# Optimization experiments

Hardware: AMD Instinct MI355X
Metric: run time of the kernel (lower is better)

The kernel has to match this reference:

```python
import jax, jax.numpy as jnp
import numpy as np

BETA = 0.25


def setup_inputs() -> dict:
    key = jax.random.key(0)
    k1, k2 = jax.random.split(key)
    x = jax.random.normal(k1, (32768, 512), dtype=jnp.float32)
    centroids = jax.random.normal(k2, (8192, 512), dtype=jnp.float32)
    return {"x": x, "centroids": centroids}


def reference(x, centroids):
    # x: [N, D], centroids: [K, D]
    x_norm = jnp.sum(x * x, axis=1, keepdims=True)          # [N, 1]
    c_norm = jnp.sum(centroids * centroids, axis=1)         # [K]
    xy = jnp.einsum('nd,kd->nk', x, centroids)              # [N, K]
    distances = x_norm + c_norm[None, :] - 2.0 * xy         # [N, K]
    indices = jnp.argmin(distances, axis=-1)                # [N]
    q = centroids[indices]                                  # [N, D] gather
    # losses: commitment = mse(sg(q), x); codebook = mse(q, sg(x))
    sg = jax.lax.stop_gradient
    commitment_loss = jnp.mean((sg(q) - x) ** 2)
    codebook_loss = jnp.mean((q - sg(x)) ** 2)
    loss = codebook_loss + BETA * commitment_loss
    # straight-through estimator
    x_q = x + sg(q - x)
    return (x_q, loss, indices)
```

## Files before the change

kernel.cpp:

```cpp
#include <hip/hip_runtime.h>
#include <hip/hip_bf16.h>

#define N_ROWS 32768
#define DIM    512
#define K_CENT 8192

#define LOSS_OFF 16777216u
#define IDX_OFF  16777217u

#define XH_OFF_B   0u
#define CH_OFF_B   33554432u
#define CN_OFF_B   41943040u
#define CAND_OFF_B 41975808u

#define BM   128
#define BN   128
#define KHALF 4096
#define NKT  (KHALF / BN)

typedef __bf16 bf16x8 __attribute__((ext_vector_type(8)));
typedef float  f32x4  __attribute__((ext_vector_type(4)));

__device__ __forceinline__ unsigned short f2bf(float f) {
    unsigned u = __float_as_uint(f);
    return (unsigned short)((u + 0x7fffu + ((u >> 16) & 1u)) >> 16);
}

__device__ __forceinline__ void glds16(void* lds, const void* g) {
    __builtin_amdgcn_global_load_lds(
        (const __attribute__((address_space(1))) unsigned*)g,
        (__attribute__((address_space(3))) unsigned*)lds, 16, 0, 0);
}

__global__ void __launch_bounds__(256) convert_kernel(const float* __restrict__ x,
                                                      const float* __restrict__ c,
                                                      unsigned short* __restrict__ xh,
                                                      unsigned short* __restrict__ ch,
                                                      float* __restrict__ cnp) {
    const int wave = threadIdx.x >> 6, lane = threadIdx.x & 63;
    const int gid = blockIdx.x * 4 + wave;
    if (gid < N_ROWS) {
        const float* p = x + (size_t)gid * DIM + lane * 8;
        float4 a = *(const float4*)p, b = *(const float4*)(p + 4);
        uint4 w;
        w.x = (unsigned)f2bf(a.x) | ((unsigned)f2bf(a.y) << 16);
        w.y = (unsigned)f2bf(a.z) | ((unsigned)f2bf(a.w) << 16);
        w.z = (unsigned)f2bf(b.x) | ((unsigned)f2bf(b.y) << 16);
        w.w = (unsigned)f2bf(b.z) | ((unsigned)f2bf(b.w) << 16);
        *(uint4*)(xh + (size_t)gid * DIM + lane * 8) = w;
    } else {
        const int cr = gid - N_ROWS;
        const float* p = c + (size_t)cr * DIM + lane * 8;
        float4 a = *(const float4*)p, b = *(const float4*)(p + 4);
        uint4 w;
        w.x = (unsigned)f2bf(a.x) | ((unsigned)f2bf(a.y) << 16);
        w.y = (unsigned)f2bf(a.z) | ((unsigned)f2bf(a.w) << 16);
        w.z = (unsigned)f2bf(b.x) | ((unsigned)f2bf(b.y) << 16);
        w.w = (unsigned)f2bf(b.z) | ((unsigned)f2bf(b.w) << 16);
        *(uint4*)(ch + (size_t)cr * DIM + lane * 8) = w;
        float s = a.x*a.x + a.y*a.y + a.z*a.z + a.w*a.w
                + b.x*b.x + b.y*b.y + b.z*b.z + b.w*b.w;
#pragma unroll
        for (int off = 32; off; off >>= 1) s += __shfl_down(s, off, 64);
        if (lane == 0) cnp[cr] = s;
    }
}

__device__ __forceinline__ void ce(float& da, int& ia, float& db, int& ib) {
    bool sw = (db < da) || (db == da && ib < ia);
    float td = sw ? db : da; int ti = sw ? ib : ia;
    float ud = sw ? da : db; int ui = sw ? ia : ib;
    da = td; ia = ti; db = ud; ib = ui;
}
__device__ __forceinline__ void lmin(float da, int ia, float db, int ib,
                                     float& od, int& oi) {
    bool sw = (db < da) || (db == da && ib < ia);
    od = sw ? db : da; oi = sw ? ib : ia;
}

__global__ void __launch_bounds__(256, 2) vq_main(const unsigned short* __restrict__ xh,
                                                  const unsigned short* __restrict__ ch,
                                                  const float* __restrict__ cnp,
                                                  float* __restrict__ cand) {
    __shared__ __align__(16) unsigned short xs[BM * 32];
    __shared__ __align__(16) unsigned short cs[BN * 32];
    __shared__ float sh_d[2][BM][4];
    __shared__ int   sh_i[2][BM][4];

    const int tid  = threadIdx.x;
    const int wave = tid >> 6, lane = tid & 63;
    const int wm   = wave >> 1, wk = wave & 1;
    const int lr   = lane & 15, quad = lane >> 4;
    const int nbase = blockIdx.x * BM;
    const int h     = blockIdx.y;
    const int kc0   = h * KHALF;

    const int srow = wave * 32 + (lane >> 2);
    const int scol = (lane & 3) * 8;
    const unsigned short* xg0 = xh + (size_t)(nbase + srow) * DIM + scol;
    unsigned short* xd0 = &xs[wave * 1024];
    unsigned short* xd1 = &xs[wave * 1024 + 512];
    unsigned short* cd0 = &cs[wave * 1024];
    unsigned short* cd1 = &cs[wave * 1024 + 512];

    int aoff[4], boff[4];
#pragma unroll
    for (int t = 0; t < 4; ++t) {
        aoff[t] = (wm * 64 + t * 16 + lr) * 32 + quad * 8;
        boff[t] = (wk * 64 + t * 16 + lr) * 32 + quad * 8;
    }

    float rd1[4][4], rd2[4][4];
    int   ri1[4][4], ri2[4][4];
#pragma unroll
    for (int mt = 0; mt < 4; ++mt)
#pragma unroll
        for (int r = 0; r < 4; ++r) {
            rd1[mt][r] = 1e30f; rd2[mt][r] = 1e30f;
            ri1[mt][r] = 0x7ffffff0; ri2[mt][r] = 0x7ffffff1;
        }

    for (int kt = 0; kt < NKT; ++kt) {
        const int kc = kc0 + kt * BN;
        const unsigned short* cg0 = ch + (size_t)(kc + srow) * DIM + scol;
        f32x4 acc[4][4];
#pragma unroll
        for (int mt = 0; mt < 4; ++mt)
#pragma unroll
            for (int t = 0; t < 4; ++t) { acc[mt][t].x = 0.f; acc[mt][t].y = 0.f; acc[mt][t].z = 0.f; acc[mt][t].w = 0.f; }

        for (int dsb = 0; dsb < 16; ++dsb) {
            const int d0 = dsb * 32;
            __syncthreads();
            glds16(xd0, xg0 + d0);
            glds16(xd1, xg0 + (size_t)16 * DIM + d0);
            glds16(cd0, cg0 + d0);
            glds16(cd1, cg0 + (size_t)16 * DIM + d0);
            __syncthreads();

            bf16x8 bfr[4];
#pragma unroll
            for (int t = 0; t < 4; ++t) bfr[t] = *(const bf16x8*)&cs[boff[t]];
#pragma unroll
            for (int mt = 0; mt < 4; ++mt) {
                bf16x8 a = *(const bf16x8*)&xs[aoff[mt]];
#pragma unroll
                for (int t = 0; t < 4; ++t)
                    acc[mt][t] = __builtin_amdgcn_mfma_f32_16x16x32_bf16(a, bfr[t], acc[mt][t], 0, 0, 0);
            }
        }

#pragma unroll
        for (int t = 0; t < 4; ++t) {
            const int col = kc + wk * 64 + t * 16 + lr;
            const float cnv = cnp[col];
#pragma unroll
            for (int mt = 0; mt < 4; ++mt)
#pragma unroll
                for (int r = 0; r < 4; ++r) {
                    float d = fmaf(-2.f, acc[mt][t][r], cnv);
                    bool b1 = d < rd1[mt][r];
                    bool b2 = d < rd2[mt][r];
                    float o1 = rd1[mt][r]; int oi1 = ri1[mt][r];
                    rd2[mt][r] = b1 ? o1 : (b2 ? d : rd2[mt][r]);
                    ri2[mt][r] = b1 ? oi1 : (b2 ? col : ri2[mt][r]);
                    rd1[mt][r] = b1 ? d : o1;
                    ri1[mt][r] = b1 ? col : oi1;
                }
        }
    }

#pragma unroll
    for (int mt = 0; mt < 4; ++mt)
#pragma unroll
        for (int r = 0; r < 4; ++r) {
            float a0 = rd1[mt][r], a1 = rd2[mt][r], a2 = 1e30f, a3 = 1e30f;
            int   i0 = ri1[mt][r], i1 = ri2[mt][r], i2 = 0x7ffffff2, i3 = 0x7ffffff3;
#pragma unroll
            for (int s = 1; s < 16; s <<= 1) {
                float p0 = __shfl_xor(a0, s, 64), p1 = __shfl_xor(a1, s, 64);
                float p2 = __shfl_xor(a2, s, 64), p3 = __shfl_xor(a3, s, 64);
                int   q0 = __shfl_xor(i0, s, 64), q1 = __shfl_xor(i1, s, 64);
                int   q2 = __shfl_xor(i2, s, 64), q3 = __shfl_xor(i3, s, 64);
                float l0, l1, l2, l3; int m0, m1, m2, m3;
                lmin(a0, i0, p3, q3, l0, m0);
                lmin(a1, i1, p2, q2, l1, m1);
                lmin(a2, i2, p1, q1, l2, m2);
                lmin(a3, i3, p0, q0, l3, m3);
                ce(l0, m0, l2, m2); ce(l1, m1, l3, m3);
                ce(l0, m0, l1, m1); ce(l2, m2, l3, m3);
                a0 = l0; a1 = l1; a2 = l2; a3 = l3;
                i0 = m0; i1 = m1; i2 = m2; i3 = m3;
            }
            if (lr == 0) {
                const int rl = wm * 64 + mt * 16 + quad * 4 + r;
                sh_d[wk][rl][0] = a0; sh_i[wk][rl][0] = i0;
                sh_d[wk][rl][1] = a1; sh_i[wk][rl][1] = i1;
                sh_d[wk][rl][2] = a2; sh_i[wk][rl][2] = i2;
                sh_d[wk][rl][3] = a3; sh_i[wk][rl][3] = i3;
            }
        }
    __syncthreads();

    if (tid < BM) {
        float a0 = sh_d[0][tid][0], a1 = sh_d[0][tid][1];
        float a2 = sh_d[0][tid][2], a3 = sh_d[0][tid][3];
        int   i0 = sh_i[0][tid][0], i1 = sh_i[0][tid][1];
        int   i2 = sh_i[0][tid][2], i3 = sh_i[0][tid][3];
        float b0 = sh_d[1][tid][0], b1 = sh_d[1][tid][1];
        float b2 = sh_d[1][tid][2], b3 = sh_d[1][tid][3];
        int   j0 = sh_i[1][tid][0], j1 = sh_i[1][tid][1];
        int   j2 = sh_i[1][tid][2], j3 = sh_i[1][tid][3];
        float l0, l1, l2, l3; int m0, m1, m2, m3;
        lmin(a0, i0, b3, j3, l0, m0);
        lmin(a1, i1, b2, j2, l1, m1);
        lmin(a2, i2, b1, j1, l2, m2);
        lmin(a3, i3, b0, j0, l3, m3);
        ce(l0, m0, l2, m2); ce(l1, m1, l3, m3);
        ce(l0, m0, l1, m1); ce(l2, m2, l3, m3);
        float* cell = cand + ((size_t)(nbase + tid) * 2 + h) * 8;
        cell[0] = l0; cell[1] = (float)m0;
        cell[2] = l1; cell[3] = (float)m1;
        cell[4] = l2; cell[5] = (float)m2;
        cell[6] = l3; cell[7] = (float)m3;
    }
}

__global__ void __launch_bounds__(256) vq_refine(const float* __restrict__ x,
                                                 const float* __restrict__ cg,
                                                 const float* __restrict__ cand,
                                                 float* __restrict__ outp) {
    __shared__ double ls[4];
    const int wave = threadIdx.x >> 6, lane = threadIdx.x & 63;
    const int n = blockIdx.x * 4 + wave;
    const float* cell = cand + (size_t)n * 16;
    int kid[8];
#pragma unroll
    for (int j = 0; j < 8; ++j) kid[j] = (int)cell[2 * j + 1];

    const float* xr = x + (size_t)n * DIM + lane * 8;
    float4 xa = *(const float4*)xr;
    float4 xb = *(const float4*)(xr + 4);

    double bd = 1e300; int bi = 0x7fffffff;
#pragma unroll
    for (int j = 0; j < 8; ++j) {
        const int k = kid[j];
        const float* cr = cg + (size_t)k * DIM + lane * 8;
        float4 ca = *(const float4*)cr;
        float4 cb = *(const float4*)(cr + 4);
        double s = 0.0, t;
        t = (double)xa.x - (double)ca.x; s += t * t;
        t = (double)xa.y - (double)ca.y; s += t * t;
        t = (double)xa.z - (double)ca.z; s += t * t;
        t = (double)xa.w - (double)ca.w; s += t * t;
        t = (double)xb.x - (double)cb.x; s += t * t;
        t = (double)xb.y - (double)cb.y; s += t * t;
        t = (double)xb.z - (double)cb.z; s += t * t;
        t = (double)xb.w - (double)cb.w; s += t * t;
#pragma unroll
        for (int off = 32; off; off >>= 1) s += __shfl_down(s, off, 64);
        s = __shfl(s, 0, 64);
        if (s < bd || (s == bd && k < bi)) { bd = s; bi = k; }
    }
    if (lane == 0) { outp[IDX_OFF + n] = (float)bi; ls[wave] = bd; }
    __syncthreads();
    if (threadIdx.x == 0)
        atomicAdd(outp + LOSS_OFF, (float)(ls[0] + ls[1] + ls[2] + ls[3]));
}

__global__ void finalize_kernel(float* __restrict__ outp) {
    if (threadIdx.x == 0) outp[LOSS_OFF] *= (1.25f / 16777216.f);
}

__global__ void __launch_bounds__(256) vq_gather(const float* __restrict__ cg,
                                                 float* __restrict__ outp) {
    const int wave = threadIdx.x >> 6, lane = threadIdx.x & 63;
    const int n = blockIdx.x * 4 + wave;
    const int k = (int)outp[IDX_OFF + n];
    const float* cr = cg + (size_t)k * DIM + lane * 8;
    float4 a = *(const float4*)cr;
    float4 b = *(const float4*)(cr + 4);
    float* row = outp + (size_t)n * DIM + lane * 8;
    *(float4*)row = a;
    *(float4*)(row + 4) = b;
}

extern "C" void kernel_launch(void* const* d_in, const int* in_sizes, int n_in,
                              void* d_out, int out_size, void* d_ws, size_t ws_size,
                              hipStream_t stream) {
    const float* x   = (const float*)d_in[0];
    const float* cen = (const float*)d_in[1];
    float* out = (float*)d_out;

    unsigned short* xh = (unsigned short*)((char*)d_out + XH_OFF_B);
    unsigned short* chp = (unsigned short*)((char*)d_out + CH_OFF_B);
    float* cnp  = (float*)((char*)d_out + CN_OFF_B);
    float* cand = (float*)((char*)d_out + CAND_OFF_B);

    hipMemsetAsync((void*)(out + LOSS_OFF), 0, sizeof(float), stream);
    convert_kernel<<<(N_ROWS + K_CENT) / 4, 256, 0, stream>>>(x, cen, xh, chp, cnp);
    dim3 g2(N_ROWS / BM, 2);
    vq_main<<<g2, 256, 0, stream>>>(xh, chp, cnp, cand);
    vq_refine<<<N_ROWS / 4, 256, 0, stream>>>(x, cen, cand, out);
    finalize_kernel<<<1, 64, 0, stream>>>(out);
    vq_gather<<<N_ROWS / 4, 256, 0, stream>>>(cen, out);
}
```

Baseline: 657.5 us.

## Widen K-step with swizzled LDS, split codebook four ways, fuse gather into refine

The distance GEMM now stages 64-wide K slices with an XOR-swizzled LDS layout, which halves the barrier count per tile and avoids bank conflicts. The codebook is split into four quarters, so the grid has more blocks, and occupancy is raised to 3 blocks per CU. Column norms are hoisted and the top-2 update uses fminf/fmaxf. The refine kernel now checks 16 candidates, writes the quantized row directly when a workspace is available, and folds loss scaling into the atomic. This drops the gather and finalize launches, at the cost of more candidate traffic and higher register pressure.

```diff
diff --git a/kernel.cpp b/kernel.cpp
--- a/kernel.cpp
+++ b/kernel.cpp
@@ -13,10 +13,15 @@
 #define CN_OFF_B   41943040u
 #define CAND_OFF_B 41975808u
 
-#define BM   128
-#define BN   128
-#define KHALF 4096
-#define NKT  (KHALF / BN)
+#define CAND_BYTES 4194304u
+#define CN_BYTES   32768u
+
+#define BM 128
+#define BN 128
+#define BK 64
+#define KQ 2048
+#define NKT (KQ / BN)
+#define NQ  (K_CENT / KQ)
 
 typedef __bf16 bf16x8 __attribute__((ext_vector_type(8)));
 typedef float  f32x4  __attribute__((ext_vector_type(4)));
@@ -30,6 +35,18 @@
     __builtin_amdgcn_global_load_lds(
         (const __attribute__((address_space(1))) unsigned*)g,
         (__attribute__((address_space(3))) unsigned*)lds, 16, 0, 0);
+}
+
+__device__ __forceinline__ void ce(float& da, int& ia, float& db, int& ib) {
+    bool sw = (db < da) || (db == da && ib < ia);
+    float td = sw ? db : da; int ti = sw ? ib : ia;
+    float ud = sw ? da : db; int ui = sw ? ia : ib;
+    da = td; ia = ti; db = ud; ib = ui;
+}
+__device__ __forceinline__ void lmin(float da, int ia, float db, int ib,
+                                     float& od, int& oi) {
+    bool sw = (db < da) || (db == da && ib < ia);
+    od = sw ? db : da; oi = sw ? ib : ia;
 }
 
 __global__ void __launch_bounds__(256) convert_kernel(const float* __restrict__ x,
@@ -66,24 +83,12 @@
     }
 }
 
-__device__ __forceinline__ void ce(float& da, int& ia, float& db, int& ib) {
-    bool sw = (db < da) || (db == da && ib < ia);
-    float td = sw ? db : da; int ti = sw ? ib : ia;
-    float ud = sw ? da : db; int ui = sw ? ia : ib;
-    da = td; ia = ti; db = ud; ib = ui;
-}
-__device__ __forceinline__ void lmin(float da, int ia, float db, int ib,
-                                     float& od, int& oi) {
-    bool sw = (db < da) || (db == da && ib < ia);
-    od = sw ? db : da; oi = sw ? ib : ia;
-}
-
-__global__ void __launch_bounds__(256, 2) vq_main(const unsigned short* __restrict__ xh,
+__global__ void __launch_bounds__(256, 3) vq_main(const unsigned short* __restrict__ xh,
                                                   const unsigned short* __restrict__ ch,
                                                   const float* __restrict__ cnp,
                                                   float* __restrict__ cand) {
-    __shared__ __align__(16) unsigned short xs[BM * 32];
-    __shared__ __align__(16) unsigned short cs[BN * 32];
+    __shared__ __align__(16) unsigned short xs[BM * BK];
+    __shared__ __align__(16) unsigned short cs[BN * BK];
     __shared__ float sh_d[2][BM][4];
     __shared__ int   sh_i[2][BM][4];
 
@@ -92,22 +97,19 @@
     const int wm   = wave >> 1, wk = wave & 1;
     const int lr   = lane & 15, quad = lane >> 4;
     const int nbase = blockIdx.x * BM;
-    const int h     = blockIdx.y;
-    const int kc0   = h * KHALF;
-
-    const int srow = wave * 32 + (lane >> 2);
-    const int scol = (lane & 3) * 8;
-    const unsigned short* xg0 = xh + (size_t)(nbase + srow) * DIM + scol;
-    unsigned short* xd0 = &xs[wave * 1024];
-    unsigned short* xd1 = &xs[wave * 1024 + 512];
-    unsigned short* cd0 = &cs[wave * 1024];
-    unsigned short* cd1 = &cs[wave * 1024 + 512];
+    const int kc0   = blockIdx.y * KQ;
+
+    const int srow8 = lane >> 3;
+    const int scol  = ((lane & 7) ^ srow8) * 8;
+    const unsigned short* xg = xh + (size_t)(nbase + wave * 32 + srow8) * DIM + scol;
+    unsigned short* xdst = xs + wave * 2048;
+    unsigned short* cdst = cs + wave * 2048;
 
     int aoff[4], boff[4];
 #pragma unroll
     for (int t = 0; t < 4; ++t) {
-        aoff[t] = (wm * 64 + t * 16 + lr) * 32 + quad * 8;
-        boff[t] = (wk * 64 + t * 16 + lr) * 32 + quad * 8;
+        aoff[t] = (wm * 64 + t * 16 + lr) * 128 + ((quad * 16) ^ ((lr & 7) << 4));
+        boff[t] = (wk * 64 + t * 16 + lr) * 128 + ((quad * 16) ^ ((lr & 7) << 4));
     }
 
     float rd1[4][4], rd2[4][4];
@@ -122,49 +124,59 @@
 
     for (int kt = 0; kt < NKT; ++kt) {
         const int kc = kc0 + kt * BN;
-        const unsigned short* cg0 = ch + (size_t)(kc + srow) * DIM + scol;
+        float cnv[4];
+#pragma unroll
+        for (int t = 0; t < 4; ++t) cnv[t] = cnp[kc + wk * 64 + t * 16 + lr];
+
+        const unsigned short* cg = ch + (size_t)(kc + wave * 32 + srow8) * DIM + scol;
+
         f32x4 acc[4][4];
 #pragma unroll
         for (int mt = 0; mt < 4; ++mt)
 #pragma unroll
-            for (int t = 0; t < 4; ++t) { acc[mt][t].x = 0.f; acc[mt][t].y = 0.f; acc[mt][t].z = 0.f; acc[mt][t].w = 0.f; }
-
-        for (int dsb = 0; dsb < 16; ++dsb) {
-            const int d0 = dsb * 32;
+            for (int t = 0; t < 4; ++t)
+                acc[mt][t] = (f32x4){0.f, 0.f, 0.f, 0.f};
+
+        for (int dsb = 0; dsb < 8; ++dsb) {
+            const int d0 = dsb * 64;
             __syncthreads();
-            glds16(xd0, xg0 + d0);
-            glds16(xd1, xg0 + (size_t)16 * DIM + d0);
-            glds16(cd0, cg0 + d0);
-            glds16(cd1, cg0 + (size_t)16 * DIM + d0);
+#pragma unroll
+            for (int g = 0; g < 4; ++g) glds16(xdst + g * 512, xg + d0 + g * 8 * DIM);
+#pragma unroll
+            for (int g = 0; g < 4; ++g) glds16(cdst + g * 512, cg + d0 + g * 8 * DIM);
             __syncthreads();
 
-            bf16x8 bfr[4];
-#pragma unroll
-            for (int t = 0; t < 4; ++t) bfr[t] = *(const bf16x8*)&cs[boff[t]];
-#pragma unroll
-            for (int mt = 0; mt < 4; ++mt) {
-                bf16x8 a = *(const bf16x8*)&xs[aoff[mt]];
+#pragma unroll
+            for (int kk = 0; kk < 2; ++kk) {
+                const int kx = kk << 6;
+                bf16x8 bfr[4];
 #pragma unroll
                 for (int t = 0; t < 4; ++t)
-                    acc[mt][t] = __builtin_amdgcn_mfma_f32_16x16x32_bf16(a, bfr[t], acc[mt][t], 0, 0, 0);
+                    bfr[t] = *(const bf16x8*)((const char*)cs + (boff[t] ^ kx));
+#pragma unroll
+                for (int mt = 0; mt < 4; ++mt) {
+                    bf16x8 a = *(const bf16x8*)((const char*)xs + (aoff[mt] ^ kx));
+#pragma unroll
+                    for (int t = 0; t < 4; ++t)
+                        acc[mt][t] = __builtin_amdgcn_mfma_f32_16x16x32_bf16(a, bfr[t], acc[mt][t], 0, 0, 0);
+                }
             }
         }
 
 #pragma unroll
         for (int t = 0; t < 4; ++t) {
             const int col = kc + wk * 64 + t * 16 + lr;
-            const float cnv = cnp[col];
 #pragma unroll
             for (int mt = 0; mt < 4; ++mt)
 #pragma unroll
                 for (int r = 0; r < 4; ++r) {
-                    float d = fmaf(-2.f, acc[mt][t][r], cnv);
-                    bool b1 = d < rd1[mt][r];
+                    float d = fmaf(-2.f, acc[mt][t][r], cnv[t]);
+                    float o1 = rd1[mt][r]; int oi1 = ri1[mt][r];
+                    bool b1 = d < o1;
                     bool b2 = d < rd2[mt][r];
-                    float o1 = rd1[mt][r]; int oi1 = ri1[mt][r];
-                    rd2[mt][r] = b1 ? o1 : (b2 ? d : rd2[mt][r]);
+                    rd2[mt][r] = fminf(fmaxf(d, o1), rd2[mt][r]);
                     ri2[mt][r] = b1 ? oi1 : (b2 ? col : ri2[mt][r]);
-                    rd1[mt][r] = b1 ? d : o1;
+                    rd1[mt][r] = fminf(d, o1);
                     ri1[mt][r] = b1 ? col : oi1;
                 }
         }
@@ -218,7 +230,7 @@
         lmin(a3, i3, b0, j0, l3, m3);
         ce(l0, m0, l2, m2); ce(l1, m1, l3, m3);
         ce(l0, m0, l1, m1); ce(l2, m2, l3, m3);
-        float* cell = cand + ((size_t)(nbase + tid) * 2 + h) * 8;
+        float* cell = cand + ((size_t)(nbase + tid) * NQ + blockIdx.y) * 8;
         cell[0] = l0; cell[1] = (float)m0;
         cell[2] = l1; cell[3] = (float)m1;
         cell[4] = l2; cell[5] = (float)m2;
@@ -229,48 +241,68 @@
 __global__ void __launch_bounds__(256) vq_refine(const float* __restrict__ x,
                                                  const float* __restrict__ cg,
                                                  const float* __restrict__ cand,
-                                                 float* __restrict__ outp) {
+                                                 float* __restrict__ outp,
+                                                 int write_xq) {
     __shared__ double ls[4];
     const int wave = threadIdx.x >> 6, lane = threadIdx.x & 63;
     const int n = blockIdx.x * 4 + wave;
-    const float* cell = cand + (size_t)n * 16;
-    int kid[8];
-#pragma unroll
-    for (int j = 0; j < 8; ++j) kid[j] = (int)cell[2 * j + 1];
+    const float* cell = cand + (size_t)n * 32;
 
     const float* xr = x + (size_t)n * DIM + lane * 8;
     float4 xa = *(const float4*)xr;
     float4 xb = *(const float4*)(xr + 4);
 
     double bd = 1e300; int bi = 0x7fffffff;
-#pragma unroll
-    for (int j = 0; j < 8; ++j) {
-        const int k = kid[j];
-        const float* cr = cg + (size_t)k * DIM + lane * 8;
-        float4 ca = *(const float4*)cr;
-        float4 cb = *(const float4*)(cr + 4);
-        double s = 0.0, t;
-        t = (double)xa.x - (double)ca.x; s += t * t;
-        t = (double)xa.y - (double)ca.y; s += t * t;
-        t = (double)xa.z - (double)ca.z; s += t * t;
-        t = (double)xa.w - (double)ca.w; s += t * t;
-        t = (double)xb.x - (double)cb.x; s += t * t;
-        t = (double)xb.y - (double)cb.y; s += t * t;
-        t = (double)xb.z - (double)cb.z; s += t * t;
-        t = (double)xb.w - (double)cb.w; s += t * t;
-#pragma unroll
-        for (int off = 32; off; off >>= 1) s += __shfl_down(s, off, 64);
-        s = __shfl(s, 0, 64);
-        if (s < bd || (s == bd && k < bi)) { bd = s; bi = k; }
+    float4 va = xa, vb = xb;
+
+#pragma unroll
+    for (int batch = 0; batch < 2; ++batch) {
+        int kid[8];
+#pragma unroll
+        for (int j = 0; j < 8; ++j) kid[j] = (int)cell[(batch * 8 + j) * 2 + 1];
+
+        float4 ca[8], cb[8];
+#pragma unroll
+        for (int j = 0; j < 8; ++j) {
+            const float* cr = cg + (size_t)kid[j] * DIM + lane * 8;
+            ca[j] = *(const float4*)cr;
+            cb[j] = *(const float4*)(cr + 4);
+        }
+
+#pragma unroll
+        for (int j = 0; j < 8; ++j) {
+            const int k = kid[j];
+            double s = 0.0, t;
+            t = (double)xa.x - (double)ca[j].x; s += t * t;
+            t = (double)xa.y - (double)ca[j].y; s += t * t;
+            t = (double)xa.z - (double)ca[j].z; s += t * t;
+            t = (double)xa.w - (double)ca[j].w; s += t * t;
+            t = (double)xb.x - (double)cb[j].x; s += t * t;
+            t = (double)xb.y - (double)cb[j].y; s += t * t;
+            t = (double)xb.z - (double)cb[j].z; s += t * t;
+            t = (double)xb.w - (double)cb[j].w; s += t * t;
+#pragma unroll
+            for (int off = 32; off; off >>= 1) s += __shfl_down(s, off, 64);
+            s = __shfl(s, 0, 64);
+            bool w = (s < bd) || (s == bd && k < bi);
+            bd = w ? s : bd;
+            bi = w ? k : bi;
+            va.x = w ? ca[j].x : va.x; va.y = w ? ca[j].y : va.y;
+            va.z = w ? ca[j].z : va.z; va.w = w ? ca[j].w : va.w;
+            vb.x = w ? cb[j].x : vb.x; vb.y = w ? cb[j].y : vb.y;
+            vb.z = w ? cb[j].z : vb.z; vb.w = w ? cb[j].w : vb.w;
+        }
+    }
+    if (write_xq) {
+        float* row = outp + (size_t)n * DIM + lane * 8;
+        *(float4*)row = va;
+        *(float4*)(row + 4) = vb;
     }
     if (lane == 0) { outp[IDX_OFF + n] = (float)bi; ls[wave] = bd; }
     __syncthreads();
     if (threadIdx.x == 0)
-        atomicAdd(outp + LOSS_OFF, (float)(ls[0] + ls[1] + ls[2] + ls[3]));
-}
-
-__global__ void finalize_kernel(float* __restrict__ outp) {
-    if (threadIdx.x == 0) outp[LOSS_OFF] *= (1.25f / 16777216.f);
+        atomicAdd(outp + LOSS_OFF,
+                  (float)((ls[0] + ls[1] + ls[2] + ls[3]) * (1.25 / 16777216.0)));
 }
 
 __global__ void __launch_bounds__(256) vq_gather(const float* __restrict__ cg,
@@ -293,16 +325,19 @@
     const float* cen = (const float*)d_in[1];
     float* out = (float*)d_out;
 
-    unsigned short* xh = (unsigned short*)((char*)d_out + XH_OFF_B);
+    unsigned short* xh  = (unsigned short*)((char*)d_out + XH_OFF_B);
     unsigned short* chp = (unsigned short*)((char*)d_out + CH_OFF_B);
-    float* cnp  = (float*)((char*)d_out + CN_OFF_B);
-    float* cand = (float*)((char*)d_out + CAND_OFF_B);
+
+    const int fused = (d_ws != nullptr) && (ws_size >= (size_t)(CAND_BYTES + CN_BYTES));
+    float* cand = fused ? (float*)d_ws
+                        : (float*)((char*)d_out + CAND_OFF_B);
+    float* cnp  = fused ? (float*)((char*)d_ws + CAND_BYTES)
+                        : (float*)((char*)d_out + CN_OFF_B);
 
     hipMemsetAsync((void*)(out + LOSS_OFF), 0, sizeof(float), stream);
     convert_kernel<<<(N_ROWS + K_CENT) / 4, 256, 0, stream>>>(x, cen, xh, chp, cnp);
-    dim3 g2(N_ROWS / BM, 2);
+    dim3 g2(N_ROWS / BM, NQ);
     vq_main<<<g2, 256, 0, stream>>>(xh, chp, cnp, cand);
-    vq_refine<<<N_ROWS / 4, 256, 0, stream>>>(x, cen, cand, out);
-    finalize_kernel<<<1, 64, 0, stream>>>(out);
-    vq_gather<<<N_ROWS / 4, 256, 0, stream>>>(cen, out);
-}
+    vq_refine<<<N_ROWS / 4, 256, 0, stream>>>(x, cen, cand, out, fused);
+    if (!fused) vq_gather<<<N_ROWS / 4, 256, 0, stream>>>(cen, out);
+}
```

Result: slower. 1.149 ms (+74.8%).
